# Optimization experiments

Hardware: AMD Instinct MI355X
Metric: run time of the kernel (lower is better)

Reference implementation:

```python
import jax, jax.numpy as jnp
import numpy as np

N = 50000
E = 800000
DIM_IN = 128
DIM_H = 16
HEADS = 8
DIM_OUT = 16
NEG_SLOPE = 0.2


def setup_inputs() -> dict:
    key = jax.random.key(0)
    ks = jax.random.split(key, 12)
    def glorot(k, shape):
        fan_in = shape[0]
        return jax.random.normal(k, shape, dtype=jnp.float32) / np.sqrt(fan_in)
    x = jax.random.normal(ks[0], (N, DIM_IN), dtype=jnp.float32)
    edge_index = jax.random.randint(ks[1], (2, E), 0, N, dtype=jnp.int64)
    # layer 1: GATv2Conv(dim_in, dim_h, heads=8)
    Wl1 = glorot(ks[2], (DIM_IN, HEADS * DIM_H))
    Wr1 = glorot(ks[3], (DIM_IN, HEADS * DIM_H))
    att1 = glorot(ks[4], (HEADS, DIM_H))
    bias1 = jnp.zeros((HEADS * DIM_H,), dtype=jnp.float32)
    # layer 2: GATv2Conv(dim_h*heads, dim_out, heads=1)
    Wl2 = glorot(ks[5], (HEADS * DIM_H, DIM_OUT))
    Wr2 = glorot(ks[6], (HEADS * DIM_H, DIM_OUT))
    att2 = glorot(ks[7], (1, DIM_OUT))
    bias2 = jnp.zeros((DIM_OUT,), dtype=jnp.float32)
    return {"x": x, "edge_index": edge_index, "Wl1": Wl1, "Wr1": Wr1,
            "att1": att1, "bias1": bias1, "Wl2": Wl2, "Wr2": Wr2,
            "att2": att2, "bias2": bias2}


def gatv2_layer(x, src, dst, Wl, Wr, att, bias, n_nodes, heads, ch):
    # x: [N, F_in]; src/dst: [Etot] (self-loops included)
    xl = (x @ Wl).reshape(n_nodes, heads, ch)  # source transform
    xr = (x @ Wr).reshape(n_nodes, heads, ch)  # target transform
    e = jax.nn.leaky_relu(xl[src] + xr[dst], NEG_SLOPE)      # [Etot, H, C]
    logits = jnp.einsum('ehc,hc->eh', e, att)                # [Etot, H]
    # segment softmax over incoming edges of each target node
    m = jax.ops.segment_max(logits, dst, num_segments=n_nodes)
    a = jnp.exp(logits - m[dst])
    denom = jax.ops.segment_sum(a, dst, num_segments=n_nodes)
    alpha = a / denom[dst]                                   # [Etot, H]
    out = jax.ops.segment_sum(xl[src] * alpha[:, :, None], dst,
                              num_segments=n_nodes)          # [N, H, C]
    return out.reshape(n_nodes, heads * ch) + bias


def reference(x, edge_index, Wl1, Wr1, att1, bias1, Wl2, Wr2, att2, bias2):
    # PyG GATv2Conv adds self-loops by default
    loops = jnp.arange(N, dtype=edge_index.dtype)
    src = jnp.concatenate([edge_index[0], loops])
    dst = jnp.concatenate([edge_index[1], loops])
    # dropout is identity in eval mode
    h = gatv2_layer(x, src, dst, Wl1, Wr1, att1, bias1, N, HEADS, DIM_H)
    h = jax.nn.elu(h)
    h = gatv2_layer(h, src, dst, Wl2, Wr2, att2, bias2, N, 1, DIM_OUT)
    return h, jax.nn.log_softmax(h, axis=1)
```

## Files before the change

kernel.cpp:

```cpp
#include <hip/hip_runtime.h>
#include <hip/hip_bf16.h>
#include <hip/hip_fp16.h>
#include <math.h>

#define NN 50000
#define EE 800000
#define DIN 128
#define HEADS 8
#define DH 16
#define DOUT 16
#define NEG 0.2f
#define GM 32
#define GB ((NN + GM - 1) / GM)
#define NB ((NN + 255) / 256)
#define ABLK ((EE / 4 + 255) / 256)
#define NPART 8
#define RANGE (NN / NPART)
#define RB 1563
#define SCATB 64
#define BUCKCAP 110000
#define PAD 64

typedef __attribute__((ext_vector_type(8))) short bf16x8;
typedef __attribute__((ext_vector_type(4))) float f32x4;
typedef __attribute__((ext_vector_type(4))) int i32x4;
typedef _Float16 h16x2 __attribute__((ext_vector_type(2)));

__device__ __forceinline__ unsigned pack2bf(float a, float b) {
    union { __hip_bfloat162 h; unsigned u; } c;
    c.h = __float22bfloat162_rn(make_float2(a, b));
    return c.u;
}
__device__ __forceinline__ unsigned short f2bf(float v) {
    union { __hip_bfloat16 h; unsigned short u; } c;
    c.h = __float2bfloat16(v);
    return c.u;
}
__device__ __forceinline__ unsigned short f2h(float v) {
    union { __half h; unsigned short u; } c;
    c.h = __float2half(v);
    return c.u;
}
__device__ __forceinline__ h16x2 u2h(unsigned u) { union { unsigned u; h16x2 h; } c; c.u = u; return c.h; }
__device__ __forceinline__ unsigned h2u(h16x2 h) { union { h16x2 h; unsigned u; } c; c.h = h; return c.u; }
__device__ __forceinline__ float h2lo(unsigned u) {
    union { unsigned short s; __half h; } c; c.s = (unsigned short)(u & 0xffffu);
    return __half2float(c.h);
}
__device__ __forceinline__ float h2hi(unsigned u) {
    union { unsigned short s; __half h; } c; c.s = (unsigned short)(u >> 16);
    return __half2float(c.h);
}
__device__ __forceinline__ float elu1(float x) { return x > 0.f ? x : __expf(x) - 1.f; }

__global__ __launch_bounds__(256) void init_bucket(int* __restrict__ cnt,
                                                   const float* __restrict__ Wl,
                                                   const float* __restrict__ Wr,
                                                   unsigned short* __restrict__ Wb,
                                                   const float* __restrict__ Wl2,
                                                   const float* __restrict__ Wr2,
                                                   unsigned short* __restrict__ Wb2,
                                                   const int* __restrict__ ei,
                                                   unsigned* __restrict__ bhead,
                                                   unsigned* __restrict__ bucket) {
    int b = blockIdx.x, t = threadIdx.x;
    if (b < NB) {
        int i = b * 256 + t;
        if (i < NN) cnt[i] = 1;
        return;
    } else if (b < NB + 128) {
        int i = (b - NB) * 256 + t;
        int n = i >> 7, k = i & 127;
        float v = (n < 128) ? Wl[k * 128 + n] : Wr[k * 128 + (n - 128)];
        Wb[i] = f2bf(v);
        return;
    } else if (b < NB + 144) {
        int i = (b - NB - 128) * 256 + t;
        int n = i >> 7, k = i & 127;
        float v = (n < 16) ? Wl2[k * 16 + n] : Wr2[k * 16 + (n - 16)];
        Wb2[i] = f2bf(v);
        return;
    }
    __shared__ unsigned lrec[1024];
    __shared__ unsigned lcnt[8], loff[8], lpos[8], gbase[8];
    int ab = b - (NB + 144);
    int i = ab * 256 + t;
    bool valid = i < EE / 4;
    i32x4 ss, dd;
    unsigned bb[4];
    if (valid) {
        ss = __builtin_nontemporal_load(((const i32x4*)ei) + i);
        dd = __builtin_nontemporal_load(((const i32x4*)(ei + EE)) + i);
    }
    if (t < 8) { lcnt[t] = 0; lpos[t] = 0; }
    __syncthreads();
    if (valid) {
#pragma unroll
        for (int e = 0; e < 4; ++e) {
            bb[e] = (unsigned)dd[e] / RANGE;
            atomicAdd(&lcnt[bb[e]], 1u);
        }
    }
    __syncthreads();
    if (t == 0) {
        unsigned run = 0;
#pragma unroll
        for (int q = 0; q < 8; ++q) { loff[q] = run; run += lcnt[q]; }
    }
    if (t < 8 && lcnt[t] > 0) gbase[t] = atomicAdd(&bhead[t], lcnt[t]);
    __syncthreads();
    if (valid) {
#pragma unroll
        for (int e = 0; e < 4; ++e) {
            unsigned p = atomicAdd(&lpos[bb[e]], 1u);
            lrec[loff[bb[e]] + p] = ((unsigned)ss[e] << 16) | (unsigned)dd[e];
        }
    }
    __syncthreads();
    unsigned total = loff[7] + lcnt[7];
    for (unsigned j = t; j < total; j += 256) {
        unsigned q = 0;
        while (q < 7 && j >= loff[q + 1]) ++q;
        bucket[(size_t)q * BUCKCAP + gbase[q] + (j - loff[q])] = lrec[j];
    }
}

__global__ __launch_bounds__(256) void scat_gemm1(const unsigned* __restrict__ bucket,
                                                  const unsigned* __restrict__ bhead,
                                                  int* __restrict__ cnt,
                                                  unsigned short* __restrict__ esrcPad,
                                                  const float* __restrict__ x,
                                                  const unsigned short* __restrict__ Wb,
                                                  unsigned short* __restrict__ xlb,
                                                  unsigned short* __restrict__ xr) {
    __shared__ unsigned short As[GM][136];
    int t = threadIdx.x;
    if (blockIdx.x < NPART * SCATB) {
        int r = blockIdx.x & 7;
        int g = blockIdx.x >> 3;
        if (g == 0) {
            for (int dq = t; dq < RANGE; dq += 256) {
                int d = r * RANGE + dq;
                esrcPad[(unsigned)d * PAD] = (unsigned short)d;
            }
        }
        unsigned n = bhead[r];
        for (unsigned i = (unsigned)g * 256 + t; i < n; i += SCATB * 256) {
            unsigned rec = __builtin_nontemporal_load(bucket + (size_t)r * BUCKCAP + i);
            unsigned s = rec >> 16, d = rec & 0xffffu;
            int p = atomicAdd(&cnt[d], 1);
            esrcPad[d * PAD + p] = (unsigned short)s;
        }
        return;
    }
    int n0 = (blockIdx.x - NPART * SCATB) * GM;
    {
        int row = t >> 3, seg = t & 7;
        int nsrc = n0 + row < NN ? n0 + row : NN - 1;
        const f32x4* xp = (const f32x4*)(x + (size_t)nsrc * DIN + 16 * seg);
        f32x4 v0 = __builtin_nontemporal_load(xp);
        f32x4 v1 = __builtin_nontemporal_load(xp + 1);
        f32x4 v2 = __builtin_nontemporal_load(xp + 2);
        f32x4 v3 = __builtin_nontemporal_load(xp + 3);
        uint4 p0 = make_uint4(pack2bf(v0[0], v0[1]), pack2bf(v0[2], v0[3]),
                              pack2bf(v1[0], v1[1]), pack2bf(v1[2], v1[3]));
        uint4 p1 = make_uint4(pack2bf(v2[0], v2[1]), pack2bf(v2[2], v2[3]),
                              pack2bf(v3[0], v3[1]), pack2bf(v3[2], v3[3]));
        *(uint4*)&As[row][16 * seg]     = p0;
        *(uint4*)&As[row][16 * seg + 8] = p1;
    }
    __syncthreads();
    int lane = t & 63, w = t >> 6;
    int m = lane & 15, quad = lane >> 4;
    f32x4 acc[2][4];
#pragma unroll
    for (int mt = 0; mt < 2; ++mt)
#pragma unroll
        for (int nt = 0; nt < 4; ++nt) acc[mt][nt] = (f32x4){0.f, 0.f, 0.f, 0.f};
#pragma unroll
    for (int ks = 0; ks < 4; ++ks) {
        int k = 32 * ks + 8 * quad;
        bf16x8 a0 = *(const bf16x8*)&As[m][k];
        bf16x8 a1 = *(const bf16x8*)&As[16 + m][k];
#pragma unroll
        for (int nt = 0; nt < 4; ++nt) {
            int n = 64 * w + 16 * nt + m;
            bf16x8 b = *(const bf16x8*)(Wb + (size_t)n * 128 + k);
            acc[0][nt] = __builtin_amdgcn_mfma_f32_16x16x32_bf16(a0, b, acc[0][nt], 0, 0, 0);
            acc[1][nt] = __builtin_amdgcn_mfma_f32_16x16x32_bf16(a1, b, acc[1][nt], 0, 0, 0);
        }
    }
    __syncthreads();
    if (w < 2) {
#pragma unroll
        for (int mt = 0; mt < 2; ++mt) {
#pragma unroll
            for (int nt = 0; nt < 4; ++nt) {
                int col = 64 * w + 16 * nt + m;
                int rbase = 16 * mt + 4 * quad;
#pragma unroll
                for (int r = 0; r < 4; ++r) As[rbase + r][col] = f2h(acc[mt][nt][r]);
            }
        }
    }
    __syncthreads();
    {
        int row = t >> 3, seg = t & 7;
        int grow = n0 + row;
        if (grow < NN) {
            uint4 a0 = *(uint4*)&As[row][16 * seg];
            uint4 a1 = *(uint4*)&As[row][16 * seg + 8];
            *(uint4*)(xlb + (unsigned)grow * DIN + 16 * seg)     = a0;
            *(uint4*)(xlb + (unsigned)grow * DIN + 16 * seg + 8) = a1;
        }
    }
    __syncthreads();
    if (w >= 2) {
#pragma unroll
        for (int mt = 0; mt < 2; ++mt) {
#pragma unroll
            for (int nt = 0; nt < 4; ++nt) {
                int col = 64 * (w - 2) + 16 * nt + m;
                int rbase = 16 * mt + 4 * quad;
#pragma unroll
                for (int r = 0; r < 4; ++r) As[rbase + r][col] = f2h(acc[mt][nt][r]);
            }
        }
    }
    __syncthreads();
    {
        int row = t >> 3, seg = t & 7;
        int grow = n0 + row;
        if (grow < NN) {
            uint4 b0 = *(uint4*)&As[row][16 * seg];
            uint4 b1 = *(uint4*)&As[row][16 * seg + 8];
            *(uint4*)(xr + (unsigned)grow * DIN + 16 * seg)     = b0;
            *(uint4*)(xr + (unsigned)grow * DIN + 16 * seg + 8) = b1;
        }
    }
}

__global__ __launch_bounds__(256) void l1_fused(const unsigned short* __restrict__ esrcPad,
                                                const int* __restrict__ cnt,
                                                const unsigned short* __restrict__ xlb,
                                                const unsigned short* __restrict__ xr,
                                                const float* __restrict__ att,
                                                const float* __restrict__ bias,
                                                unsigned short* __restrict__ hb) {
    int r = blockIdx.x & 7;
    int dq = (blockIdx.x >> 3) * 4 + (threadIdx.x >> 6);
    if (dq >= RANGE) return;
    int d = r * RANGE + dq;
    int lane = threadIdx.x & 63;
    int quarter = lane >> 4;
    int q16 = lane & 15;
    int rs = d * PAD;
    int re = rs + cnt[d];
    int last = re - 1;
    uint4 xru = ((const uint4*)(xr + (unsigned)d * DIN))[q16];
    h16x2 xh0 = u2h(xru.x), xh1 = u2h(xru.y), xh2 = u2h(xru.z), xh3 = u2h(xru.w);
    float4 at0 = ((const float4*)att)[2 * q16];
    float4 at1 = ((const float4*)att)[2 * q16 + 1];
    h16x2 ah0 = (h16x2){(_Float16)at0.x, (_Float16)at0.y};
    h16x2 ah1 = (h16x2){(_Float16)at0.z, (_Float16)at0.w};
    h16x2 ah2 = (h16x2){(_Float16)at1.x, (_Float16)at1.y};
    h16x2 ah3 = (h16x2){(_Float16)at1.z, (_Float16)at1.w};
    const h16x2 c06 = (h16x2){(_Float16)0.6f, (_Float16)0.6f};
    const h16x2 c04 = (h16x2){(_Float16)0.4f, (_Float16)0.4f};
    float4 a0 = make_float4(0.f, 0.f, 0.f, 0.f);
    float4 a1 = make_float4(0.f, 0.f, 0.f, 0.f);
    float l = 0.f;
    int slot = rs + quarter;
    int c0i = slot < last ? slot : last;
    unsigned s0 = esrcPad[c0i];
    int c1i = slot + 4 < last ? slot + 4 : last;
    unsigned s1 = esrcPad[c1i];
    uint4 row = ((const uint4*)(xlb + s0 * (unsigned)DIN))[q16];
    for (; slot < re; slot += 4) {
        uint4 cur = row;
        int c2i = slot + 8 < last ? slot + 8 : last;
        unsigned s2 = esrcPad[c2i];
        row = ((const uint4*)(xlb + s1 * (unsigned)DIN))[q16];
        s1 = s2;
        h16x2 c0 = u2h(cur.x), c1 = u2h(cur.y), c2 = u2h(cur.z), c3 = u2h(cur.w);
        h16x2 v0 = c0 + xh0, v1 = c1 + xh1, v2 = c2 + xh2, v3 = c3 + xh3;
        h16x2 w0 = v0 * c06 + u2h(h2u(v0) & 0x7fff7fffu) * c04;
        h16x2 w1 = v1 * c06 + u2h(h2u(v1) & 0x7fff7fffu) * c04;
        h16x2 w2 = v2 * c06 + u2h(h2u(v2) & 0x7fff7fffu) * c04;
        h16x2 w3 = v3 * c06 + u2h(h2u(v3) & 0x7fff7fffu) * c04;
        float w = __builtin_amdgcn_fdot2(w0, ah0, 0.f, false);
        w = __builtin_amdgcn_fdot2(w1, ah1, w, false);
        w = __builtin_amdgcn_fdot2(w2, ah2, w, false);
        w = __builtin_amdgcn_fdot2(w3, ah3, w, false);
        w += __shfl_xor(w, 1);
        float p = __expf(w);
        a0.x += p * (float)c0[0]; a0.y += p * (float)c0[1];
        a0.z += p * (float)c1[0]; a0.w += p * (float)c1[1];
        a1.x += p * (float)c2[0]; a1.y += p * (float)c2[1];
        a1.z += p * (float)c3[0]; a1.w += p * (float)c3[1];
        l += p;
    }
#pragma unroll
    for (int off = 16; off < 64; off <<= 1) {
        a0.x += __shfl_xor(a0.x, off); a0.y += __shfl_xor(a0.y, off);
        a0.z += __shfl_xor(a0.z, off); a0.w += __shfl_xor(a0.w, off);
        a1.x += __shfl_xor(a1.x, off); a1.y += __shfl_xor(a1.y, off);
        a1.z += __shfl_xor(a1.z, off); a1.w += __shfl_xor(a1.w, off);
        l += __shfl_xor(l, off);
    }
    if (quarter == 0) {
        float inv = 1.f / l;
        float4 b0 = ((const float4*)bias)[2 * q16];
        float4 b1 = ((const float4*)bias)[2 * q16 + 1];
        float4 o0, o1;
        o0.x = elu1(a0.x * inv + b0.x);
        o0.y = elu1(a0.y * inv + b0.y);
        o0.z = elu1(a0.z * inv + b0.z);
        o0.w = elu1(a0.w * inv + b0.w);
        o1.x = elu1(a1.x * inv + b1.x);
        o1.y = elu1(a1.y * inv + b1.y);
        o1.z = elu1(a1.z * inv + b1.z);
        o1.w = elu1(a1.w * inv + b1.w);
        uint4 pk = make_uint4(pack2bf(o0.x, o0.y), pack2bf(o0.z, o0.w),
                              pack2bf(o1.x, o1.y), pack2bf(o1.z, o1.w));
        ((uint4*)(hb + (unsigned)d * DIN))[q16] = pk;
    }
}

__global__ __launch_bounds__(256) void gemm2(const unsigned short* __restrict__ hb,
                                             const unsigned short* __restrict__ Wb2,
                                             unsigned short* __restrict__ xlr2) {
    __shared__ unsigned short As[GM][136];
    int t = threadIdx.x;
    int n0 = blockIdx.x * GM;
    {
        int row = t >> 3, s8 = t & 7;
        int nsrc = n0 + row < NN ? n0 + row : NN - 1;
        const uint4* src = (const uint4*)(hb + (size_t)nsrc * DIN);
        *(uint4*)&As[row][8 * s8]      = src[s8];
        *(uint4*)&As[row][8 * s8 + 64] = src[s8 + 8];
    }
    __syncthreads();
    int lane = t & 63, w = t >> 6;
    int m = lane & 15, quad = lane >> 4;
    int mt = w & 1, nt = w >> 1;
    f32x4 acc = (f32x4){0.f, 0.f, 0.f, 0.f};
#pragma unroll
    for (int ks = 0; ks < 4; ++ks) {
        int k = 32 * ks + 8 * quad;
        bf16x8 a = *(const bf16x8*)&As[16 * mt + m][k];
        bf16x8 b = *(const bf16x8*)(Wb2 + (size_t)(16 * nt + m) * 128 + k);
        acc = __builtin_amdgcn_mfma_f32_16x16x32_bf16(a, b, acc, 0, 0, 0);
    }
#pragma unroll
    for (int r = 0; r < 4; ++r) {
        int node = n0 + 16 * mt + 4 * quad + r;
        if (node < NN) xlr2[(unsigned)node * 32 + nt * 16 + m] = f2h(acc[r]);
    }
}

__global__ __launch_bounds__(256) void l2_fused(const unsigned short* __restrict__ esrcPad,
                                                const int* __restrict__ cnt,
                                                const unsigned short* __restrict__ xlr2,
                                                const float* __restrict__ att,
                                                const float* __restrict__ bias,
                                                float* __restrict__ out) {
    int r = blockIdx.x & 7;
    int dq = (blockIdx.x >> 3) * 4 + (threadIdx.x >> 6);
    if (dq >= RANGE) return;
    int d = r * RANGE + dq;
    int lane = threadIdx.x & 63;
    int sl = lane >> 2;
    int q = lane & 3;
    int rs = d * PAD;
    int re = rs + cnt[d];
    int last = re - 1;
    uint2 xr2u = *(const uint2*)(xlr2 + (unsigned)d * 32 + 16 + 4 * q);
    float4 xrq;
    xrq.x = h2lo(xr2u.x); xrq.y = h2hi(xr2u.x);
    xrq.z = h2lo(xr2u.y); xrq.w = h2hi(xr2u.y);
    float4 atq = ((const float4*)att)[q];
    float4 acc = make_float4(0.f, 0.f, 0.f, 0.f);
    float l = 0.f;
    int slot = rs + sl;
    int c0 = slot < last ? slot : last;
    unsigned s0 = esrcPad[c0];
    for (; slot < re; slot += 16) {
        int c1 = slot + 16 < last ? slot + 16 : last;
        unsigned s1 = esrcPad[c1];
        uint2 cu = *(const uint2*)(xlr2 + s0 * 32u + 4u * q);
        s0 = s1;
        float4 cur;
        cur.x = h2lo(cu.x); cur.y = h2hi(cu.x);
        cur.z = h2lo(cu.y); cur.w = h2hi(cu.y);
        float v0 = cur.x + xrq.x; v0 = fmaxf(v0, NEG * v0);
        float v1 = cur.y + xrq.y; v1 = fmaxf(v1, NEG * v1);
        float v2 = cur.z + xrq.z; v2 = fmaxf(v2, NEG * v2);
        float v3 = cur.w + xrq.w; v3 = fmaxf(v3, NEG * v3);
        float w = atq.x * v0 + atq.y * v1 + atq.z * v2 + atq.w * v3;
        w += __shfl_xor(w, 1);
        w += __shfl_xor(w, 2);
        float p = __expf(w);
        acc.x += p * cur.x; acc.y += p * cur.y;
        acc.z += p * cur.z; acc.w += p * cur.w;
        l += p;
    }
#pragma unroll
    for (int off = 4; off < 64; off <<= 1) {
        acc.x += __shfl_xor(acc.x, off);
        acc.y += __shfl_xor(acc.y, off);
        acc.z += __shfl_xor(acc.z, off);
        acc.w += __shfl_xor(acc.w, off);
        l += __shfl_xor(l, off);
    }
    float inv = 1.f / l;
    float4 b = ((const float4*)bias)[q];
    float4 v;
    v.x = acc.x * inv + b.x; v.y = acc.y * inv + b.y;
    v.z = acc.z * inv + b.z; v.w = acc.w * inv + b.w;
    float m = fmaxf(fmaxf(v.x, v.y), fmaxf(v.z, v.w));
    m = fmaxf(m, __shfl_xor(m, 1));
    m = fmaxf(m, __shfl_xor(m, 2));
    float es = __expf(v.x - m) + __expf(v.y - m) + __expf(v.z - m) + __expf(v.w - m);
    es += __shfl_xor(es, 1);
    es += __shfl_xor(es, 2);
    float lse = m + __logf(es);
    if (sl == 0) {
        ((float4*)(out + (size_t)d * DOUT))[q] = v;
        float4 ls;
        ls.x = v.x - lse; ls.y = v.y - lse; ls.z = v.z - lse; ls.w = v.w - lse;
        ((float4*)(out + (size_t)NN * DOUT + (size_t)d * DOUT))[q] = ls;
    }
}

extern "C" void kernel_launch(void* const* d_in, const int* in_sizes, int n_in,
                              void* d_out, int out_size, void* d_ws, size_t ws_size,
                              hipStream_t stream) {
    const float* x     = (const float*)d_in[0];
    const int*   ei    = (const int*)d_in[1];
    const float* Wl1   = (const float*)d_in[2];
    const float* Wr1   = (const float*)d_in[3];
    const float* att1  = (const float*)d_in[4];
    const float* bias1 = (const float*)d_in[5];
    const float* Wl2   = (const float*)d_in[6];
    const float* Wr2   = (const float*)d_in[7];
    const float* att2  = (const float*)d_in[8];
    const float* bias2 = (const float*)d_in[9];
    float* out = (float*)d_out;

    unsigned short* xr1 = (unsigned short*)d_ws;
    unsigned short* xlr2 = xr1 + (size_t)NN * DIN;
    unsigned short* xlb = xlr2 + (size_t)NN * 32;
    unsigned short* hb  = xlb + (size_t)NN * DIN;
    unsigned short* Wb  = hb + (size_t)NN * DIN;
    unsigned short* Wb2 = Wb + 256 * 128;
    unsigned short* esrcPad = Wb2 + 32 * 128;
    int*   cnt    = (int*)(esrcPad + (size_t)NN * PAD);
    unsigned* bucket = (unsigned*)(cnt + NN);
    unsigned* bhead  = bucket + (size_t)8 * BUCKCAP;

    const int B = 256;
    hipMemsetAsync(bhead, 0, 8 * sizeof(unsigned), stream);
    init_bucket<<<NB + 144 + ABLK, B, 0, stream>>>(cnt, Wl1, Wr1, Wb, Wl2, Wr2, Wb2,
                                                   ei, bhead, bucket);
    scat_gemm1<<<NPART * SCATB + GB, B, 0, stream>>>(bucket, bhead, cnt, esrcPad,
                                                     x, Wb, xlb, xr1);
    l1_fused<<<NPART * RB, B, 0, stream>>>(esrcPad, cnt, xlb, xr1, att1, bias1, hb);
    gemm2<<<GB, B, 0, stream>>>(hb, Wb2, xlr2);
    l2_fused<<<NPART * RB, B, 0, stream>>>(esrcPad, cnt, xlr2, att2, bias2, out);
}
```

Measured before the change: 225.3 us.

## Deepen gather prefetch in layer-1 aggregation and zero counts via memset

The layer-1 edge loop now keeps three source rows in flight instead of one or two, to hide the latency of gathered loads. The per-node count array is now cleared with a memset rather than set to one in a kernel, and the count semantics are shifted by one (self-loop implicit) in the scatter and both aggregation kernels. The scatter phase also gets twice as many blocks per partition. The deeper prefetch costs extra registers and may reduce occupancy.

```diff
diff --git a/kernel.cpp b/kernel.cpp
--- a/kernel.cpp
+++ b/kernel.cpp
@@ -12,12 +12,11 @@
 #define NEG 0.2f
 #define GM 32
 #define GB ((NN + GM - 1) / GM)
-#define NB ((NN + 255) / 256)
 #define ABLK ((EE / 4 + 255) / 256)
 #define NPART 8
 #define RANGE (NN / NPART)
 #define RB 1563
-#define SCATB 64
+#define SCATB 128
 #define BUCKCAP 110000
 #define PAD 64
 
@@ -53,8 +52,7 @@
 }
 __device__ __forceinline__ float elu1(float x) { return x > 0.f ? x : __expf(x) - 1.f; }
 
-__global__ __launch_bounds__(256) void init_bucket(int* __restrict__ cnt,
-                                                   const float* __restrict__ Wl,
+__global__ __launch_bounds__(256) void init_bucket(const float* __restrict__ Wl,
                                                    const float* __restrict__ Wr,
                                                    unsigned short* __restrict__ Wb,
                                                    const float* __restrict__ Wl2,
@@ -64,18 +62,14 @@
                                                    unsigned* __restrict__ bhead,
                                                    unsigned* __restrict__ bucket) {
     int b = blockIdx.x, t = threadIdx.x;
-    if (b < NB) {
+    if (b < 128) {
         int i = b * 256 + t;
-        if (i < NN) cnt[i] = 1;
-        return;
-    } else if (b < NB + 128) {
-        int i = (b - NB) * 256 + t;
         int n = i >> 7, k = i & 127;
         float v = (n < 128) ? Wl[k * 128 + n] : Wr[k * 128 + (n - 128)];
         Wb[i] = f2bf(v);
         return;
-    } else if (b < NB + 144) {
-        int i = (b - NB - 128) * 256 + t;
+    } else if (b < 144) {
+        int i = (b - 128) * 256 + t;
         int n = i >> 7, k = i & 127;
         float v = (n < 16) ? Wl2[k * 16 + n] : Wr2[k * 16 + (n - 16)];
         Wb2[i] = f2bf(v);
@@ -83,7 +77,7 @@
     }
     __shared__ unsigned lrec[1024];
     __shared__ unsigned lcnt[8], loff[8], lpos[8], gbase[8];
-    int ab = b - (NB + 144);
+    int ab = b - 144;
     int i = ab * 256 + t;
     bool valid = i < EE / 4;
     i32x4 ss, dd;
@@ -148,7 +142,7 @@
         for (unsigned i = (unsigned)g * 256 + t; i < n; i += SCATB * 256) {
             unsigned rec = __builtin_nontemporal_load(bucket + (size_t)r * BUCKCAP + i);
             unsigned s = rec >> 16, d = rec & 0xffffu;
-            int p = atomicAdd(&cnt[d], 1);
+            int p = atomicAdd(&cnt[d], 1) + 1;
             esrcPad[d * PAD + p] = (unsigned short)s;
         }
         return;
@@ -255,7 +249,7 @@
     int quarter = lane >> 4;
     int q16 = lane & 15;
     int rs = d * PAD;
-    int re = rs + cnt[d];
+    int re = rs + 1 + cnt[d];
     int last = re - 1;
     uint4 xru = ((const uint4*)(xr + (unsigned)d * DIN))[q16];
     h16x2 xh0 = u2h(xru.x), xh1 = u2h(xru.y), xh2 = u2h(xru.z), xh3 = u2h(xru.w);
@@ -271,17 +265,20 @@
     float4 a1 = make_float4(0.f, 0.f, 0.f, 0.f);
     float l = 0.f;
     int slot = rs + quarter;
-    int c0i = slot < last ? slot : last;
-    unsigned s0 = esrcPad[c0i];
-    int c1i = slot + 4 < last ? slot + 4 : last;
-    unsigned s1 = esrcPad[c1i];
-    uint4 row = ((const uint4*)(xlb + s0 * (unsigned)DIN))[q16];
+    int cA = slot < last ? slot : last;
+    int cB = slot + 4 < last ? slot + 4 : last;
+    int cC = slot + 8 < last ? slot + 8 : last;
+    unsigned sA = esrcPad[cA], sB = esrcPad[cB], sC = esrcPad[cC];
+    uint4 rowA = ((const uint4*)(xlb + sA * (unsigned)DIN))[q16];
+    uint4 rowB = ((const uint4*)(xlb + sB * (unsigned)DIN))[q16];
+    uint4 rowC = ((const uint4*)(xlb + sC * (unsigned)DIN))[q16];
     for (; slot < re; slot += 4) {
-        uint4 cur = row;
-        int c2i = slot + 8 < last ? slot + 8 : last;
-        unsigned s2 = esrcPad[c2i];
-        row = ((const uint4*)(xlb + s1 * (unsigned)DIN))[q16];
-        s1 = s2;
+        uint4 cur = rowA;
+        rowA = rowB;
+        rowB = rowC;
+        int cD = slot + 12 < last ? slot + 12 : last;
+        unsigned sD = esrcPad[cD];
+        rowC = ((const uint4*)(xlb + sD * (unsigned)DIN))[q16];
         h16x2 c0 = u2h(cur.x), c1 = u2h(cur.y), c2 = u2h(cur.z), c3 = u2h(cur.w);
         h16x2 v0 = c0 + xh0, v1 = c1 + xh1, v2 = c2 + xh2, v3 = c3 + xh3;
         h16x2 w0 = v0 * c06 + u2h(h2u(v0) & 0x7fff7fffu) * c04;
@@ -373,7 +370,7 @@
     int sl = lane >> 2;
     int q = lane & 3;
     int rs = d * PAD;
-    int re = rs + cnt[d];
+    int re = rs + 1 + cnt[d];
     int last = re - 1;
     uint2 xr2u = *(const uint2*)(xlr2 + (unsigned)d * 32 + 16 + 4 * q);
     float4 xrq;
@@ -460,9 +457,10 @@
     unsigned* bhead  = bucket + (size_t)8 * BUCKCAP;
 
     const int B = 256;
+    hipMemsetAsync(cnt, 0, NN * sizeof(int), stream);
     hipMemsetAsync(bhead, 0, 8 * sizeof(unsigned), stream);
-    init_bucket<<<NB + 144 + ABLK, B, 0, stream>>>(cnt, Wl1, Wr1, Wb, Wl2, Wr2, Wb2,
-                                                   ei, bhead, bucket);
+    init_bucket<<<144 + ABLK, B, 0, stream>>>(Wl1, Wr1, Wb, Wl2, Wr2, Wb2,
+                                              ei, bhead, bucket);
     scat_gemm1<<<NPART * SCATB + GB, B, 0, stream>>>(bucket, bhead, cnt, esrcPad,
                                                      x, Wb, xlb, xr1);
     l1_fused<<<NPART * RB, B, 0, stream>>>(esrcPad, cnt, xlb, xr1, att1, bias1, hb);
```

New measurement: 231.8 us. 1.03x slower.
